# Kernel optimization log

Measured on AMD Instinct MI355X. Metric: run time of the kernel, lower is better.

## Reference

```python
import jax, jax.numpy as jnp
import numpy as np

D_MODEL = 2048
HIDDEN = 2048
NUM_EXPERTS = 8
TOP_K = 2
CAPACITY_FACTOR = 1.25


def setup_inputs() -> dict:
    key = jax.random.key(0)
    k1, k2, k3, k4, k5, k6 = jax.random.split(key, 6)
    N = 8192
    x = jax.random.normal(k1, (N, D_MODEL), dtype=jnp.float32)
    expert_weights = jax.random.uniform(k2, (N, TOP_K), dtype=jnp.float32)
    expert_indices = jax.random.randint(k3, (N, TOP_K), 0, NUM_EXPERTS)
    scale = 0.02
    w1 = jax.random.normal(k4, (NUM_EXPERTS, D_MODEL, HIDDEN), dtype=jnp.float32) * scale
    w3 = jax.random.normal(k5, (NUM_EXPERTS, D_MODEL, HIDDEN), dtype=jnp.float32) * scale
    w2 = jax.random.normal(k6, (NUM_EXPERTS, HIDDEN, D_MODEL), dtype=jnp.float32) * scale
    return {"x": x, "expert_weights": expert_weights, "expert_indices": expert_indices,
            "w1": w1, "w2": w2, "w3": w3}


def reference(x, expert_weights, expert_indices, w1, w2, w3):
    N, top_k = expert_weights.shape
    E = NUM_EXPERTS
    d = x.shape[-1]
    capacity = int(CAPACITY_FACTOR * top_k * N / E)  # expert_capacity()

    flat_idx = expert_indices.reshape(-1)            # (T,) T = N*top_k
    flat_w = expert_weights.reshape(-1)
    T = flat_idx.shape[0]

    # indices_and_bins: histogram + sort (jnp.argsort is stable)
    counts = jax.ops.segment_sum(jnp.ones((T,), dtype=jnp.int32), flat_idx, num_segments=E)
    order = jnp.argsort(flat_idx)                    # sorted assignment order
    sorted_e = flat_idx[order]                       # expert id per sorted slot
    starts = jnp.concatenate([jnp.zeros((1,), jnp.int32), jnp.cumsum(counts)[:-1].astype(jnp.int32)])
    off = jnp.arange(T, dtype=jnp.int32) - starts[sorted_e]  # position within expert bin
    valid = off < capacity                           # capacity dropping
    off_c = jnp.where(valid, off, 0)
    tok = order // top_k                             # source token per assignment

    # binned_gather -> (E, capacity, d); dropped/unfilled slots are zero
    xg = jnp.zeros((E, capacity, d), dtype=x.dtype)
    xg = xg.at[sorted_e, off_c].add(x[tok] * valid[:, None].astype(x.dtype))

    # per-expert SwiGLU MLP (grouped GEMMs)
    h = jax.nn.silu(jnp.einsum('ecd,edh->ech', xg, w1)) * jnp.einsum('ecd,edh->ech', xg, w3)
    y = jnp.einsum('ech,ehd->ecd', h, w2)

    # binned_scatter with expert_weights (weighted combine back to tokens)
    vals = y[sorted_e, off_c] * (flat_w[order] * valid.astype(x.dtype))[:, None]
    out = jnp.zeros((N, d), dtype=x.dtype).at[tok].add(vals)
    return out, counts
```

## Files before the change

### kernel.cpp

```cpp
#include <hip/hip_runtime.h>
#include <hip/hip_bf16.h>
#include <stdint.h>

#define NTOK 8192
#define DM 2048
#define DH 2048
#define NEXP 8
#define TOPK 2
#define TASSIGN (NTOK * TOPK)
#define CAP 2560
#define MROWS (NEXP * CAP)
#define BMTILES 10
#define RBLK 64

using bf16x8 = __attribute__((ext_vector_type(8))) __bf16;
using f32x4  = __attribute__((ext_vector_type(4))) float;

__device__ __forceinline__ void load_lds16(const void* g, void* l) {
    __builtin_amdgcn_global_load_lds((const __attribute__((address_space(1))) void*)g,
                                     (__attribute__((address_space(3))) void*)l,
                                     16, 0, 0);
}

__global__ void route_hist_kernel(const int* __restrict__ eidx,
                                  int* __restrict__ chunk_cnt,
                                  int* __restrict__ slot_token)
{
    int b = blockIdx.x, tid = threadIdx.x, lane = tid & 63, wid = tid >> 6;
    __shared__ int wcnt[4][NEXP];
    for (int i = b * 320 + tid; i < (b + 1) * 320; i += 256) slot_token[i] = -1;
    int e = eidx[b * 256 + tid];
    #pragma unroll
    for (int ex = 0; ex < NEXP; ex++) {
        unsigned long long m = __ballot(e == ex);
        if (lane == 0) wcnt[wid][ex] = __popcll(m);
    }
    __syncthreads();
    if (tid < NEXP) {
        int s = 0;
        #pragma unroll
        for (int w = 0; w < 4; w++) s += wcnt[w][tid];
        chunk_cnt[b * NEXP + tid] = s;
    }
}

__global__ void route_scan_kernel(const int* __restrict__ chunk_cnt,
                                  int* __restrict__ chunk_base,
                                  int* __restrict__ counts,
                                  float* __restrict__ counts_out)
{
    int e = threadIdx.x;
    if (e < NEXP) {
        int run = 0;
        for (int b = 0; b < RBLK; b++) {
            chunk_base[b * NEXP + e] = run;
            run += chunk_cnt[b * NEXP + e];
        }
        counts[e] = run;
        counts_out[e] = (float)run;
    }
}

__global__ void route_assign_kernel(const int* __restrict__ eidx,
                                    const int* __restrict__ chunk_base,
                                    int* __restrict__ slot_token,
                                    int* __restrict__ assign_slot)
{
    int b = blockIdx.x, tid = threadIdx.x, lane = tid & 63, wid = tid >> 6;
    __shared__ int wcnt[4][NEXP];
    int t = b * 256 + tid;
    int e = eidx[t];
    unsigned long long mymask = 0;
    #pragma unroll
    for (int ex = 0; ex < NEXP; ex++) {
        unsigned long long m = __ballot(e == ex);
        if (ex == e) mymask = m;
        if (lane == 0) wcnt[wid][ex] = __popcll(m);
    }
    int rankw = __popcll(mymask & ((1ull << lane) - 1ull));
    __syncthreads();
    int r = chunk_base[b * NEXP + e] + rankw;
    for (int w = 0; w < wid; w++) r += wcnt[w][e];
    int slot = (r < CAP) ? (e * CAP + r) : -1;
    assign_slot[t] = slot;
    if (slot >= 0) slot_token[slot] = t >> 1;
}

__global__ void transpose_kernel(const float* __restrict__ wa,
                                 const float* __restrict__ wb,
                                 const float* __restrict__ wc,
                                 __bf16* __restrict__ wat,
                                 __bf16* __restrict__ wbt,
                                 __bf16* __restrict__ wct)
{
    __shared__ float tile[64][65];
    int z = blockIdx.z;
    int mat = z >> 3, e = z & 7;
    const float* src = (mat == 0 ? wa : mat == 1 ? wb : wc) + (size_t)e * DM * DH;
    __bf16* dst = (mat == 0 ? wat : mat == 1 ? wbt : wct) + (size_t)e * DM * DH;
    int k0 = blockIdx.x * 64, n0 = blockIdx.y * 64;
    int tid = threadIdx.x;
    #pragma unroll
    for (int i = 0; i < 16; i++) {
        int lin = tid + i * 256;
        int r = lin >> 6, c = lin & 63;
        tile[r][c] = src[(size_t)(k0 + r) * DH + (n0 + c)];
    }
    __syncthreads();
    #pragma unroll
    for (int i = 0; i < 2; i++) {
        int rn = (tid >> 3) + i * 32;
        int ck = (tid & 7) * 8;
        bf16x8 v;
        #pragma unroll
        for (int j = 0; j < 8; j++) v[j] = (__bf16)tile[ck + j][rn];
        *(bf16x8*)(dst + (size_t)(n0 + rn) * DM + (k0 + ck)) = v;
    }
}

__global__ void gather_kernel(const float* __restrict__ x,
                              const int* __restrict__ slot_token,
                              __bf16* __restrict__ xg)
{
    int slot = blockIdx.x;
    int tok = slot_token[slot];
    int c = threadIdx.x * 8;
    float f[8];
    if (tok >= 0) {
        const float4* px = (const float4*)(x + (size_t)tok * DM + c);
        float4 a = px[0], b = px[1];
        f[0] = a.x; f[1] = a.y; f[2] = a.z; f[3] = a.w;
        f[4] = b.x; f[5] = b.y; f[6] = b.z; f[7] = b.w;
    } else {
        #pragma unroll
        for (int i = 0; i < 8; i++) f[i] = 0.f;
    }
    bf16x8 v;
    #pragma unroll
    for (int i = 0; i < 8; i++) v[i] = (__bf16)f[i];
    *(bf16x8*)(xg + (size_t)slot * DM + c) = v;
}

template<bool FUSED>
__global__ __launch_bounds__(512, 2)
void gemm8_kernel(const __bf16* __restrict__ A,
                  const __bf16* __restrict__ B1,
                  const __bf16* __restrict__ B2,
                  __bf16* __restrict__ C,
                  const int* __restrict__ counts)
{
    constexpr int K = 2048, N = 2048;
    constexpr int BM = 256;
    constexpr int BN = FUSED ? 128 : 256;
    constexpr int NTILES = N / BN;
    constexpr int NT = K / 64;
    constexpr int NJ = FUSED ? 2 : 4;
    constexpr int ROWB = K * 2;

    extern __shared__ char smem[];

    constexpr int PERE = BMTILES * NTILES;
    constexpr int PERX = NEXP * PERE / 8;
    int w = (blockIdx.x % 8) * PERX + blockIdx.x / 8;
    int e = w / PERE;
    int r = w % PERE;
    int ntg = r / (BMTILES * 4);
    int rr  = r % (BMTILES * 4);
    int ntile = ntg * 4 + rr / BMTILES;
    int mtile = rr % BMTILES;

    int mloc = mtile * BM;
    int rows = counts[e]; if (rows > CAP) rows = CAP;
    if (mloc >= rows) return;

    int tid = threadIdx.x;
    int wid = tid >> 6, lane = tid & 63;
    int wm = wid & 1, wn = wid >> 1;
    size_t rowBase = (size_t)e * CAP + mloc;

    int r0 = tid >> 3;
    int sw = ((tid & 7) ^ (r0 & 7)) << 4;
    const char* sA = (const char*)(A + (rowBase + r0) * (size_t)K) + sw;
    const char* sBu0; const char* sBu1;
    {
        size_t brow = (size_t)e * N + (size_t)ntile * BN + r0;
        sBu0 = (const char*)(B1 + brow * (size_t)K) + sw;
        if constexpr (FUSED) sBu1 = (const char*)(B2 + brow * (size_t)K) + sw;
        else                 sBu1 = sBu0 + 128 * ROWB;
    }
    char* lw = smem + wid * 1024;

    auto stage2 = [&](const char* s, int koff, int ldsOff) {
        load_lds16(s + koff, lw + ldsOff);
        load_lds16(s + koff + 64 * ROWB, lw + ldsOff + 8192);
    };

    int xc0 = (((lane >> 4) + 0) ^ (lane & 7)) << 4;
    int xc1 = (((lane >> 4) + 4) ^ (lane & 7)) << 4;
    int aOff = (wm * 128 + (lane & 15)) * 128;
    int bOff1, bOff2 = 0;
    if constexpr (FUSED) {
        bOff1 = 32768 + (wn * 32 + (lane & 15)) * 128;
        bOff2 = bOff1 + 16384;
    } else {
        bOff1 = 32768 + (wn * 64 + (lane & 15)) * 128;
    }

    f32x4 acc1[8][NJ];
    f32x4 acc2[FUSED ? 8 : 1][NJ];
    #pragma unroll
    for (int i = 0; i < 8; i++)
        #pragma unroll
        for (int j = 0; j < NJ; j++) {
            acc1[i][j] = (f32x4){0.f, 0.f, 0.f, 0.f};
            if constexpr (FUSED) acc2[i][j] = (f32x4){0.f, 0.f, 0.f, 0.f};
        }

    stage2(sA,              0, 0);
    stage2(sA + 128 * ROWB, 0, 16384);
    stage2(sBu0,            0, 32768);
    stage2(sBu1,            0, 49152);
    stage2(sBu0,          128, 65536 + 32768);
    stage2(sBu1,          128, 65536 + 49152);
    asm volatile("s_waitcnt vmcnt(4)" ::: "memory");
    __builtin_amdgcn_sched_barrier(0);
    __builtin_amdgcn_s_barrier();

    bf16x8 b1f[NJ][2];
    bf16x8 b2f[FUSED ? NJ : 1][2];

    #pragma unroll 2
    for (int t = 0; t < NT; ++t) {
        int bufC = (t & 1) << 16;
        int bufO = bufC ^ 65536;
        #pragma unroll
        for (int p = 0; p < 4; ++p) {
            bf16x8 a[2][2];
            #pragma unroll
            for (int i2 = 0; i2 < 2; ++i2) {
                const char* ap = smem + bufC + aOff + (2 * p + i2) * 2048;
                a[i2][0] = *(const bf16x8*)(ap + xc0);
                a[i2][1] = *(const bf16x8*)(ap + xc1);
            }
            if (p == 0) {
                #pragma unroll
                for (int j = 0; j < NJ; ++j) {
                    const char* bp = smem + bufC + bOff1 + j * 2048;
                    b1f[j][0] = *(const bf16x8*)(bp + xc0);
                    b1f[j][1] = *(const bf16x8*)(bp + xc1);
                    if constexpr (FUSED) {
                        const char* bp2 = smem + bufC + bOff2 + j * 2048;
                        b2f[j][0] = *(const bf16x8*)(bp2 + xc0);
                        b2f[j][1] = *(const bf16x8*)(bp2 + xc1);
                    }
                }
            }
            if (p == 0) {
                if (t + 1 < NT) {
                    stage2(sA,              (t + 1) * 128, bufO);
                    stage2(sA + 128 * ROWB, (t + 1) * 128, bufO + 16384);
                }
            } else if (p == 1) { if (t + 2 < NT) stage2(sBu0, (t + 2) * 128, bufC + 32768); }
            else if (p == 2)   { if (t + 2 < NT) stage2(sBu1, (t + 2) * 128, bufC + 49152); }

            __builtin_amdgcn_s_barrier();
            asm volatile("s_waitcnt lgkmcnt(0)" ::: "memory");
            __builtin_amdgcn_sched_barrier(0);
            __builtin_amdgcn_s_setprio(1);
            #pragma unroll
            for (int ks = 0; ks < 2; ++ks)
                #pragma unroll
                for (int i2 = 0; i2 < 2; ++i2)
                    #pragma unroll
                    for (int j = 0; j < NJ; ++j) {
                        acc1[2 * p + i2][j] = __builtin_amdgcn_mfma_f32_16x16x32_bf16(
                            a[i2][ks], b1f[j][ks], acc1[2 * p + i2][j], 0, 0, 0);
                        if constexpr (FUSED)
                            acc2[2 * p + i2][j] = __builtin_amdgcn_mfma_f32_16x16x32_bf16(
                                a[i2][ks], b2f[j][ks], acc2[2 * p + i2][j], 0, 0, 0);
                    }
            __builtin_amdgcn_s_setprio(0);
            __builtin_amdgcn_sched_barrier(0);
            if (p == 3) {
                if (t + 2 < NT)      { asm volatile("s_waitcnt vmcnt(4)" ::: "memory"); }
                else if (t + 1 < NT) { asm volatile("s_waitcnt vmcnt(0)" ::: "memory"); }
                __builtin_amdgcn_sched_barrier(0);
            }
            __builtin_amdgcn_s_barrier();
        }
    }

    size_t crow0 = rowBase + wm * 128 + ((lane >> 4) << 2);
    int col0 = ntile * BN + wn * (FUSED ? 32 : 64) + (lane & 15);
    #pragma unroll
    for (int i = 0; i < 8; ++i)
        #pragma unroll
        for (int j = 0; j < NJ; ++j)
            #pragma unroll
            for (int r4 = 0; r4 < 4; ++r4) {
                float v = acc1[i][j][r4];
                if constexpr (FUSED) {
                    float z3 = acc2[i][j][r4];
                    v = (v / (1.f + __expf(-v))) * z3;
                }
                C[(crow0 + i * 16 + r4) * (size_t)N + (col0 + j * 16)] = (__bf16)v;
            }
}

__global__ void combine_kernel(const __bf16* __restrict__ y,
                               const int* __restrict__ assign_slot,
                               const float* __restrict__ ew,
                               float* __restrict__ out)
{
    int n = blockIdx.x;
    int s0 = assign_slot[2 * n], s1 = assign_slot[2 * n + 1];
    float w0 = ew[2 * n], w1 = ew[2 * n + 1];
    int c = threadIdx.x * 8;
    float acc[8];
    #pragma unroll
    for (int i = 0; i < 8; i++) acc[i] = 0.f;
    if (s0 >= 0) {
        bf16x8 v = *(const bf16x8*)(y + (size_t)s0 * DM + c);
        #pragma unroll
        for (int i = 0; i < 8; i++) acc[i] += w0 * (float)v[i];
    }
    if (s1 >= 0) {
        bf16x8 v = *(const bf16x8*)(y + (size_t)s1 * DM + c);
        #pragma unroll
        for (int i = 0; i < 8; i++) acc[i] += w1 * (float)v[i];
    }
    float4* po = (float4*)(out + (size_t)n * DM + c);
    po[0] = (float4){acc[0], acc[1], acc[2], acc[3]};
    po[1] = (float4){acc[4], acc[5], acc[6], acc[7]};
}

extern "C" void kernel_launch(void* const* d_in, const int* in_sizes, int n_in,
                              void* d_out, int out_size, void* d_ws, size_t ws_size,
                              hipStream_t stream)
{
    const float* x  = (const float*)d_in[0];
    const float* ew = (const float*)d_in[1];
    const int* eidx = (const int*)d_in[2];
    const float* w1 = (const float*)d_in[3];
    const float* w2 = (const float*)d_in[4];
    const float* w3 = (const float*)d_in[5];
    float* out = (float*)d_out;
    float* counts_out = out + (size_t)NTOK * DM;

    char* ws = (char*)d_ws;
    size_t off = 0;
    auto alloc = [&](size_t bytes) -> void* {
        off = (off + 255) & ~(size_t)255;
        void* p = ws + off;
        off += bytes;
        return p;
    };
    int* slot_token  = (int*)alloc((size_t)MROWS * 4);
    int* assign_slot = (int*)alloc((size_t)TASSIGN * 4);
    int* counts      = (int*)alloc(NEXP * 4);
    int* chunk_cnt   = (int*)alloc((size_t)RBLK * NEXP * 4);
    int* chunk_base  = (int*)alloc((size_t)RBLK * NEXP * 4);
    __bf16* xg  = (__bf16*)alloc((size_t)MROWS * DM * 2);
    __bf16* h   = (__bf16*)alloc((size_t)MROWS * DH * 2);
    __bf16* w1t = (__bf16*)alloc((size_t)NEXP * DM * DH * 2);
    __bf16* w3t = (__bf16*)alloc((size_t)NEXP * DM * DH * 2);
    __bf16* w2t = (__bf16*)alloc((size_t)NEXP * DM * DH * 2);
    __bf16* y = xg;

    static int attr_done = 0;
    if (!attr_done) {
        hipFuncSetAttribute((const void*)gemm8_kernel<true>,
                            hipFuncAttributeMaxDynamicSharedMemorySize, 131072);
        hipFuncSetAttribute((const void*)gemm8_kernel<false>,
                            hipFuncAttributeMaxDynamicSharedMemorySize, 131072);
        attr_done = 1;
    }

    route_hist_kernel<<<RBLK, 256, 0, stream>>>(eidx, chunk_cnt, slot_token);
    route_scan_kernel<<<1, 64, 0, stream>>>(chunk_cnt, chunk_base, counts, counts_out);
    route_assign_kernel<<<RBLK, 256, 0, stream>>>(eidx, chunk_base, slot_token, assign_slot);
    transpose_kernel<<<dim3(32, 32, 24), 256, 0, stream>>>(w1, w3, w2, w1t, w3t, w2t);
    gather_kernel<<<MROWS, 256, 0, stream>>>(x, slot_token, xg);
    gemm8_kernel<true><<<NEXP * BMTILES * 16, 512, 131072, stream>>>(xg, w1t, w3t, h, counts);
    gemm8_kernel<false><<<NEXP * BMTILES * 8, 512, 131072, stream>>>(h, w2t, nullptr, y, counts);
    combine_kernel<<<NTOK, 256, 0, stream>>>(y, assign_slot, ew, out);
}
```

Before: 923.1 us.

## Restructure GEMM k-loop into four phases; shrink down-projection tile to 128 columns

The fused gate/up GEMM's inner k-loop is reorganized into four half-tile phases that interleave LDS fragment reads, global-to-LDS staging and MFMA bursts, instead of the earlier four-pass layout with all B fragments loaded up front. The down-projection GEMM now uses BN=128 (twice as many blocks) with a simpler two-phase loop and fewer outstanding loads. The goals are lower register pressure, better overlap of loads with MFMA work, and more parallelism in the second GEMM. The cost is that A tiles are re-read more often for the second GEMM and fewer FLOPs run per staged byte.

```diff
diff --git a/kernel.cpp b/kernel.cpp
--- a/kernel.cpp
+++ b/kernel.cpp
@@ -150,11 +150,9 @@
                   const int* __restrict__ counts)
 {
     constexpr int K = 2048, N = 2048;
-    constexpr int BM = 256;
-    constexpr int BN = FUSED ? 128 : 256;
+    constexpr int BM = 256, BN = 128;
     constexpr int NTILES = N / BN;
     constexpr int NT = K / 64;
-    constexpr int NJ = FUSED ? 2 : 4;
     constexpr int ROWB = K * 2;
 
     extern __shared__ char smem[];
@@ -181,13 +179,9 @@
     int r0 = tid >> 3;
     int sw = ((tid & 7) ^ (r0 & 7)) << 4;
     const char* sA = (const char*)(A + (rowBase + r0) * (size_t)K) + sw;
-    const char* sBu0; const char* sBu1;
-    {
-        size_t brow = (size_t)e * N + (size_t)ntile * BN + r0;
-        sBu0 = (const char*)(B1 + brow * (size_t)K) + sw;
-        if constexpr (FUSED) sBu1 = (const char*)(B2 + brow * (size_t)K) + sw;
-        else                 sBu1 = sBu0 + 128 * ROWB;
-    }
+    size_t brow = (size_t)e * N + (size_t)ntile * BN + r0;
+    const char* sBu0 = (const char*)(B1 + brow * (size_t)K) + sw;
+    const char* sBu1 = FUSED ? (const char*)(B2 + brow * (size_t)K) + sw : nullptr;
     char* lw = smem + wid * 1024;
 
     auto stage2 = [&](const char* s, int koff, int ldsOff) {
@@ -198,20 +192,15 @@
     int xc0 = (((lane >> 4) + 0) ^ (lane & 7)) << 4;
     int xc1 = (((lane >> 4) + 4) ^ (lane & 7)) << 4;
     int aOff = (wm * 128 + (lane & 15)) * 128;
-    int bOff1, bOff2 = 0;
-    if constexpr (FUSED) {
-        bOff1 = 32768 + (wn * 32 + (lane & 15)) * 128;
-        bOff2 = bOff1 + 16384;
-    } else {
-        bOff1 = 32768 + (wn * 64 + (lane & 15)) * 128;
-    }
-
-    f32x4 acc1[8][NJ];
-    f32x4 acc2[FUSED ? 8 : 1][NJ];
+    int bOff1 = 32768 + (wn * 32 + (lane & 15)) * 128;
+    int bOff2 = bOff1 + 16384;
+
+    f32x4 acc1[8][2];
+    f32x4 acc2[FUSED ? 8 : 1][2];
     #pragma unroll
     for (int i = 0; i < 8; i++)
         #pragma unroll
-        for (int j = 0; j < NJ; j++) {
+        for (int j = 0; j < 2; j++) {
             acc1[i][j] = (f32x4){0.f, 0.f, 0.f, 0.f};
             if constexpr (FUSED) acc2[i][j] = (f32x4){0.f, 0.f, 0.f, 0.f};
         }
@@ -219,83 +208,152 @@
     stage2(sA,              0, 0);
     stage2(sA + 128 * ROWB, 0, 16384);
     stage2(sBu0,            0, 32768);
-    stage2(sBu1,            0, 49152);
-    stage2(sBu0,          128, 65536 + 32768);
-    stage2(sBu1,          128, 65536 + 49152);
-    asm volatile("s_waitcnt vmcnt(4)" ::: "memory");
+    if constexpr (FUSED) {
+        stage2(sBu1,   0, 49152);
+        stage2(sBu0, 128, 65536 + 32768);
+        stage2(sBu1, 128, 65536 + 49152);
+        asm volatile("s_waitcnt vmcnt(4)" ::: "memory");
+    } else {
+        stage2(sBu0, 128, 65536 + 32768);
+        asm volatile("s_waitcnt vmcnt(2)" ::: "memory");
+    }
     __builtin_amdgcn_sched_barrier(0);
     __builtin_amdgcn_s_barrier();
-
-    bf16x8 b1f[NJ][2];
-    bf16x8 b2f[FUSED ? NJ : 1][2];
 
     #pragma unroll 2
     for (int t = 0; t < NT; ++t) {
         int bufC = (t & 1) << 16;
         int bufO = bufC ^ 65536;
-        #pragma unroll
-        for (int p = 0; p < 4; ++p) {
-            bf16x8 a[2][2];
-            #pragma unroll
-            for (int i2 = 0; i2 < 2; ++i2) {
-                const char* ap = smem + bufC + aOff + (2 * p + i2) * 2048;
-                a[i2][0] = *(const bf16x8*)(ap + xc0);
-                a[i2][1] = *(const bf16x8*)(ap + xc1);
-            }
-            if (p == 0) {
-                #pragma unroll
-                for (int j = 0; j < NJ; ++j) {
-                    const char* bp = smem + bufC + bOff1 + j * 2048;
-                    b1f[j][0] = *(const bf16x8*)(bp + xc0);
-                    b1f[j][1] = *(const bf16x8*)(bp + xc1);
-                    if constexpr (FUSED) {
-                        const char* bp2 = smem + bufC + bOff2 + j * 2048;
-                        b2f[j][0] = *(const bf16x8*)(bp2 + xc0);
-                        b2f[j][1] = *(const bf16x8*)(bp2 + xc1);
-                    }
-                }
-            }
-            if (p == 0) {
-                if (t + 1 < NT) {
-                    stage2(sA,              (t + 1) * 128, bufO);
-                    stage2(sA + 128 * ROWB, (t + 1) * 128, bufO + 16384);
-                }
-            } else if (p == 1) { if (t + 2 < NT) stage2(sBu0, (t + 2) * 128, bufC + 32768); }
-            else if (p == 2)   { if (t + 2 < NT) stage2(sBu1, (t + 2) * 128, bufC + 49152); }
-
-            __builtin_amdgcn_s_barrier();
-            asm volatile("s_waitcnt lgkmcnt(0)" ::: "memory");
-            __builtin_amdgcn_sched_barrier(0);
-            __builtin_amdgcn_s_setprio(1);
-            #pragma unroll
-            for (int ks = 0; ks < 2; ++ks)
-                #pragma unroll
-                for (int i2 = 0; i2 < 2; ++i2)
-                    #pragma unroll
-                    for (int j = 0; j < NJ; ++j) {
-                        acc1[2 * p + i2][j] = __builtin_amdgcn_mfma_f32_16x16x32_bf16(
-                            a[i2][ks], b1f[j][ks], acc1[2 * p + i2][j], 0, 0, 0);
-                        if constexpr (FUSED)
-                            acc2[2 * p + i2][j] = __builtin_amdgcn_mfma_f32_16x16x32_bf16(
-                                a[i2][ks], b2f[j][ks], acc2[2 * p + i2][j], 0, 0, 0);
-                    }
-            __builtin_amdgcn_s_setprio(0);
-            __builtin_amdgcn_sched_barrier(0);
-            if (p == 3) {
-                if (t + 2 < NT)      { asm volatile("s_waitcnt vmcnt(4)" ::: "memory"); }
-                else if (t + 1 < NT) { asm volatile("s_waitcnt vmcnt(0)" ::: "memory"); }
-                __builtin_amdgcn_sched_barrier(0);
-            }
+        const char* base = smem + bufC;
+
+        if constexpr (FUSED) {
+            bf16x8 a0[4], a1[4], bkA[4], bkB[4];
+            #pragma unroll
+            for (int i = 0; i < 4; i++) a0[i] = *(const bf16x8*)(base + aOff + i * 2048 + xc0);
+            bkA[0] = *(const bf16x8*)(base + bOff1 + 0    + xc0);
+            bkA[1] = *(const bf16x8*)(base + bOff1 + 2048 + xc0);
+            bkA[2] = *(const bf16x8*)(base + bOff2 + 0    + xc0);
+            bkA[3] = *(const bf16x8*)(base + bOff2 + 2048 + xc0);
+            if (t + 1 < NT) stage2(sA, (t + 1) * 128, bufO);
+            asm volatile("s_waitcnt lgkmcnt(0)" ::: "memory");
+            __builtin_amdgcn_sched_barrier(0);
+            __builtin_amdgcn_s_setprio(1);
+            #pragma unroll
+            for (int i = 0; i < 4; i++) {
+                acc1[i][0] = __builtin_amdgcn_mfma_f32_16x16x32_bf16(a0[i], bkA[0], acc1[i][0], 0, 0, 0);
+                acc1[i][1] = __builtin_amdgcn_mfma_f32_16x16x32_bf16(a0[i], bkA[1], acc1[i][1], 0, 0, 0);
+                acc2[i][0] = __builtin_amdgcn_mfma_f32_16x16x32_bf16(a0[i], bkA[2], acc2[i][0], 0, 0, 0);
+                acc2[i][1] = __builtin_amdgcn_mfma_f32_16x16x32_bf16(a0[i], bkA[3], acc2[i][1], 0, 0, 0);
+            }
+            __builtin_amdgcn_s_setprio(0);
+            __builtin_amdgcn_sched_barrier(0);
+            __builtin_amdgcn_s_barrier();
+            #pragma unroll
+            for (int i = 0; i < 4; i++) a1[i] = *(const bf16x8*)(base + aOff + (4 + i) * 2048 + xc0);
+            bkB[0] = *(const bf16x8*)(base + bOff1 + 0    + xc1);
+            bkB[1] = *(const bf16x8*)(base + bOff1 + 2048 + xc1);
+            bkB[2] = *(const bf16x8*)(base + bOff2 + 0    + xc1);
+            bkB[3] = *(const bf16x8*)(base + bOff2 + 2048 + xc1);
+            if (t + 1 < NT) stage2(sA + 128 * ROWB, (t + 1) * 128, bufO + 16384);
+            asm volatile("s_waitcnt lgkmcnt(0)" ::: "memory");
+            __builtin_amdgcn_sched_barrier(0);
+            __builtin_amdgcn_s_setprio(1);
+            #pragma unroll
+            for (int i = 0; i < 4; i++) {
+                acc1[4 + i][0] = __builtin_amdgcn_mfma_f32_16x16x32_bf16(a1[i], bkA[0], acc1[4 + i][0], 0, 0, 0);
+                acc1[4 + i][1] = __builtin_amdgcn_mfma_f32_16x16x32_bf16(a1[i], bkA[1], acc1[4 + i][1], 0, 0, 0);
+                acc2[4 + i][0] = __builtin_amdgcn_mfma_f32_16x16x32_bf16(a1[i], bkA[2], acc2[4 + i][0], 0, 0, 0);
+                acc2[4 + i][1] = __builtin_amdgcn_mfma_f32_16x16x32_bf16(a1[i], bkA[3], acc2[4 + i][1], 0, 0, 0);
+            }
+            __builtin_amdgcn_s_setprio(0);
+            __builtin_amdgcn_sched_barrier(0);
+            __builtin_amdgcn_s_barrier();
+            #pragma unroll
+            for (int i = 0; i < 4; i++) a0[i] = *(const bf16x8*)(base + aOff + i * 2048 + xc1);
+            asm volatile("s_waitcnt lgkmcnt(0)" ::: "memory");
+            __builtin_amdgcn_sched_barrier(0);
+            __builtin_amdgcn_s_setprio(1);
+            #pragma unroll
+            for (int i = 0; i < 4; i++) {
+                acc1[i][0] = __builtin_amdgcn_mfma_f32_16x16x32_bf16(a0[i], bkB[0], acc1[i][0], 0, 0, 0);
+                acc1[i][1] = __builtin_amdgcn_mfma_f32_16x16x32_bf16(a0[i], bkB[1], acc1[i][1], 0, 0, 0);
+                acc2[i][0] = __builtin_amdgcn_mfma_f32_16x16x32_bf16(a0[i], bkB[2], acc2[i][0], 0, 0, 0);
+                acc2[i][1] = __builtin_amdgcn_mfma_f32_16x16x32_bf16(a0[i], bkB[3], acc2[i][1], 0, 0, 0);
+            }
+            __builtin_amdgcn_s_setprio(0);
+            __builtin_amdgcn_sched_barrier(0);
+            __builtin_amdgcn_s_barrier();
+            #pragma unroll
+            for (int i = 0; i < 4; i++) a1[i] = *(const bf16x8*)(base + aOff + (4 + i) * 2048 + xc1);
+            if (t + 2 < NT) {
+                stage2(sBu0, (t + 2) * 128, bufC + 32768);
+                stage2(sBu1, (t + 2) * 128, bufC + 49152);
+            }
+            asm volatile("s_waitcnt lgkmcnt(0)" ::: "memory");
+            __builtin_amdgcn_sched_barrier(0);
+            __builtin_amdgcn_s_setprio(1);
+            #pragma unroll
+            for (int i = 0; i < 4; i++) {
+                acc1[4 + i][0] = __builtin_amdgcn_mfma_f32_16x16x32_bf16(a1[i], bkB[0], acc1[4 + i][0], 0, 0, 0);
+                acc1[4 + i][1] = __builtin_amdgcn_mfma_f32_16x16x32_bf16(a1[i], bkB[1], acc1[4 + i][1], 0, 0, 0);
+                acc2[4 + i][0] = __builtin_amdgcn_mfma_f32_16x16x32_bf16(a1[i], bkB[2], acc2[4 + i][0], 0, 0, 0);
+                acc2[4 + i][1] = __builtin_amdgcn_mfma_f32_16x16x32_bf16(a1[i], bkB[3], acc2[4 + i][1], 0, 0, 0);
+            }
+            __builtin_amdgcn_s_setprio(0);
+            __builtin_amdgcn_sched_barrier(0);
+            if (t + 2 < NT)      { asm volatile("s_waitcnt vmcnt(4)" ::: "memory"); }
+            else if (t + 1 < NT) { asm volatile("s_waitcnt vmcnt(0)" ::: "memory"); }
+            __builtin_amdgcn_sched_barrier(0);
+            __builtin_amdgcn_s_barrier();
+        } else {
+            bf16x8 a0[8], bk0[2], bk1[2];
+            #pragma unroll
+            for (int i = 0; i < 8; i++) a0[i] = *(const bf16x8*)(base + aOff + i * 2048 + xc0);
+            bk0[0] = *(const bf16x8*)(base + bOff1 + 0    + xc0);
+            bk0[1] = *(const bf16x8*)(base + bOff1 + 2048 + xc0);
+            bk1[0] = *(const bf16x8*)(base + bOff1 + 0    + xc1);
+            bk1[1] = *(const bf16x8*)(base + bOff1 + 2048 + xc1);
+            if (t + 1 < NT) {
+                stage2(sA,              (t + 1) * 128, bufO);
+                stage2(sA + 128 * ROWB, (t + 1) * 128, bufO + 16384);
+            }
+            asm volatile("s_waitcnt lgkmcnt(0)" ::: "memory");
+            __builtin_amdgcn_sched_barrier(0);
+            __builtin_amdgcn_s_setprio(1);
+            #pragma unroll
+            for (int i = 0; i < 8; i++) {
+                acc1[i][0] = __builtin_amdgcn_mfma_f32_16x16x32_bf16(a0[i], bk0[0], acc1[i][0], 0, 0, 0);
+                acc1[i][1] = __builtin_amdgcn_mfma_f32_16x16x32_bf16(a0[i], bk0[1], acc1[i][1], 0, 0, 0);
+            }
+            __builtin_amdgcn_s_setprio(0);
+            __builtin_amdgcn_sched_barrier(0);
+            __builtin_amdgcn_s_barrier();
+            #pragma unroll
+            for (int i = 0; i < 8; i++) a0[i] = *(const bf16x8*)(base + aOff + i * 2048 + xc1);
+            if (t + 2 < NT) stage2(sBu0, (t + 2) * 128, bufC + 32768);
+            asm volatile("s_waitcnt lgkmcnt(0)" ::: "memory");
+            __builtin_amdgcn_sched_barrier(0);
+            __builtin_amdgcn_s_setprio(1);
+            #pragma unroll
+            for (int i = 0; i < 8; i++) {
+                acc1[i][0] = __builtin_amdgcn_mfma_f32_16x16x32_bf16(a0[i], bk1[0], acc1[i][0], 0, 0, 0);
+                acc1[i][1] = __builtin_amdgcn_mfma_f32_16x16x32_bf16(a0[i], bk1[1], acc1[i][1], 0, 0, 0);
+            }
+            __builtin_amdgcn_s_setprio(0);
+            __builtin_amdgcn_sched_barrier(0);
+            if (t + 2 < NT)      { asm volatile("s_waitcnt vmcnt(2)" ::: "memory"); }
+            else if (t + 1 < NT) { asm volatile("s_waitcnt vmcnt(0)" ::: "memory"); }
+            __builtin_amdgcn_sched_barrier(0);
             __builtin_amdgcn_s_barrier();
         }
     }
 
     size_t crow0 = rowBase + wm * 128 + ((lane >> 4) << 2);
-    int col0 = ntile * BN + wn * (FUSED ? 32 : 64) + (lane & 15);
+    int col0 = ntile * BN + wn * 32 + (lane & 15);
     #pragma unroll
     for (int i = 0; i < 8; ++i)
         #pragma unroll
-        for (int j = 0; j < NJ; ++j)
+        for (int j = 0; j < 2; ++j)
             #pragma unroll
             for (int r4 = 0; r4 < 4; ++r4) {
                 float v = acc1[i][j][r4];
@@ -382,6 +440,6 @@
     transpose_kernel<<<dim3(32, 32, 24), 256, 0, stream>>>(w1, w3, w2, w1t, w3t, w2t);
     gather_kernel<<<MROWS, 256, 0, stream>>>(x, slot_token, xg);
     gemm8_kernel<true><<<NEXP * BMTILES * 16, 512, 131072, stream>>>(xg, w1t, w3t, h, counts);
-    gemm8_kernel<false><<<NEXP * BMTILES * 8, 512, 131072, stream>>>(h, w2t, nullptr, y, counts);
+    gemm8_kernel<false><<<NEXP * BMTILES * 16, 512, 131072, stream>>>(h, w2t, nullptr, y, counts);
     combine_kernel<<<NTOK, 256, 0, stream>>>(y, assign_slot, ew, out);
 }
```

After: 906.2 us. About the same (-1.8%).
